# Performance work log

Measured on AMD Instinct MI355X. Metric: run time of the kernel, lower is better.

## Reference

```python
import jax, jax.numpy as jnp
import numpy as np

N = 50000      # nodes
E = 400000     # edges (before self-loops)
F = 128        # num_features
H = 8          # heads
C = 64         # hidden_channels (per-head dim of conv1)
K = 32         # num_classes (per-head dim of conv2)
NEG_SLOPE = 0.2


def _glorot(key, shape):
    fan_in, fan_out = shape[0], shape[-1]
    scale = jnp.sqrt(2.0 / (fan_in + fan_out)).astype(jnp.float32)
    return jax.random.normal(key, shape, dtype=jnp.float32) * scale


def setup_inputs() -> dict:
    key = jax.random.key(0)
    ks = jax.random.split(key, 14)
    return {
        "x": jax.random.normal(ks[0], (N, F), dtype=jnp.float32),
        "edge_index": jax.random.randint(ks[1], (2, E), 0, N, dtype=jnp.int32),
        "xyz": jax.random.normal(ks[2], (N, 3), dtype=jnp.float32),
        # lin1 residual: Linear(F, K)
        "lin1_w": _glorot(ks[3], (F, K)),
        "lin1_b": jnp.zeros((K,), jnp.float32),
        # conv1: GATv2Conv(F, C, heads=8, concat=False)
        "wl1": _glorot(ks[4], (F, H * C)),
        "wr1": _glorot(ks[5], (F, H * C)),
        "att1": _glorot(ks[6], (H, C)),
        "b1": jnp.zeros((C,), jnp.float32),
        # conv2: GATv2Conv(C, K, heads=8, concat=False)
        "wl2": _glorot(ks[7], (C, H * K)),
        "wr2": _glorot(ks[8], (C, H * K)),
        "att2": _glorot(ks[9], (H, K)),
        "b2": jnp.zeros((K,), jnp.float32),
    }


def _gatv2_layer(x, src, dst, wl, wr, att, bias, heads, ch):
    """GATv2Conv with concat=False (mean over heads), add_self_loops already in edges."""
    n = x.shape[0]
    xl = (x @ wl).reshape(n, heads, ch)   # source transform W_l x
    xr = (x @ wr).reshape(n, heads, ch)   # target transform W_r x
    # edge score: e_ij = a_h . leaky_relu(xl[j] + xr[i])  -> [E, H]
    e = jnp.einsum('ehc,hc->eh', jax.nn.leaky_relu(xl[src] + xr[dst], NEG_SLOPE), att)
    # segment softmax over incoming edges of each destination node
    m = jax.ops.segment_max(e, dst, num_segments=n)
    ex = jnp.exp(e - m[dst])
    denom = jax.ops.segment_sum(ex, dst, num_segments=n)
    alpha = ex / denom[dst]                                      # [E, H]
    out = jax.ops.segment_sum(alpha[:, :, None] * xl[src], dst, num_segments=n)  # [N, H, C]
    return out.mean(axis=1) + bias        # concat=False -> head average, then bias


def reference(x, edge_index, xyz, lin1_w, lin1_b, wl1, wr1, att1, b1,
              wl2, wr2, att2, b2):
    n = x.shape[0]
    # PyG GATv2Conv default: add self loops
    loops = jnp.arange(n, dtype=edge_index.dtype)
    src = jnp.concatenate([edge_index[0], loops])
    dst = jnp.concatenate([edge_index[1], loops])

    residual1 = x @ lin1_w + lin1_b                      # lin1(x)
    h = _gatv2_layer(x, src, dst, wl1, wr1, att1, b1, H, C)
    h = jax.nn.relu(h)                                   # dropout is identity in eval
    out = _gatv2_layer(h, src, dst, wl2, wr2, att2, b2, H, K)
    return out + residual1
```

## Files before the change

kernel.cpp:

```cpp
#include <hip/hip_runtime.h>
#include <hip/hip_bf16.h>

#define NNODE 50000
#define NEDGE 400000
#define NTOT  450000
#define FDIM  128
#define HEADS 8
#define SCANB ((NNODE + 255) / 256)

typedef __bf16 bf16x8 __attribute__((ext_vector_type(8)));
typedef float  f32x4  __attribute__((ext_vector_type(4)));
typedef unsigned short u16x8 __attribute__((ext_vector_type(8)));
typedef unsigned short u16x4 __attribute__((ext_vector_type(4)));
typedef __hip_bfloat16 bf16;

static __device__ __forceinline__ float lrelu(float v) {
  return v > 0.f ? v : 0.2f * v;
}
static __device__ __forceinline__ float b2f(unsigned short u) {
  union { float f; unsigned int i; } x; x.i = ((unsigned int)u) << 16; return x.f;
}


__global__ __launch_bounds__(256) void k_count(const int* __restrict__ ei, int* __restrict__ deg) {
  int t = blockIdx.x * 256 + threadIdx.x;
  if (t >= NTOT) return;
  int d = (t < NEDGE) ? ei[NEDGE + t] : (t - NEDGE);
  atomicAdd(&deg[d], 1);
}

__global__ __launch_bounds__(256) void k_scan1(const int* __restrict__ deg, int* __restrict__ offs,
                                               int* __restrict__ bsum) {
  __shared__ int buf[256];
  int i = blockIdx.x * 256 + threadIdx.x;
  int v = (i < NNODE) ? deg[i] : 0;
  buf[threadIdx.x] = v;
  __syncthreads();
  for (int off = 1; off < 256; off <<= 1) {
    int t = (threadIdx.x >= off) ? buf[threadIdx.x - off] : 0;
    __syncthreads();
    buf[threadIdx.x] += t;
    __syncthreads();
  }
  if (i < NNODE) offs[i + 1] = buf[threadIdx.x];
  if (threadIdx.x == 255) bsum[blockIdx.x] = buf[255];
  if (i == 0) offs[0] = 0;
}

__global__ __launch_bounds__(256) void k_scan2(int* __restrict__ bsum, int nb) {
  __shared__ int buf[256];
  int v = (threadIdx.x < nb) ? bsum[threadIdx.x] : 0;
  buf[threadIdx.x] = v;
  __syncthreads();
  for (int off = 1; off < 256; off <<= 1) {
    int t = (threadIdx.x >= off) ? buf[threadIdx.x - off] : 0;
    __syncthreads();
    buf[threadIdx.x] += t;
    __syncthreads();
  }
  if (threadIdx.x < nb) bsum[threadIdx.x] = buf[threadIdx.x] - v;
}

__global__ __launch_bounds__(256) void k_scan3(int* __restrict__ offs, const int* __restrict__ bsum) {
  int i = blockIdx.x * 256 + threadIdx.x;
  if (i < NNODE) offs[i + 1] += bsum[blockIdx.x];
}

__global__ __launch_bounds__(256) void k_fill(const int* __restrict__ ei, const int* __restrict__ offs,
                                              int* __restrict__ cur, int* __restrict__ csrc) {
  int t = blockIdx.x * 256 + threadIdx.x;
  if (t >= NTOT) return;
  int s, d;
  if (t < NEDGE) { s = ei[t]; d = ei[NEDGE + t]; }
  else { s = t - NEDGE; d = s; }
  int pos = offs[d] + atomicAdd(&cur[d], 1);
  csrc[pos] = s;
}


__global__ __launch_bounds__(256) void k_cast(const float* __restrict__ in, bf16* __restrict__ o, int nvec) {
  int t = blockIdx.x * 256 + threadIdx.x;
  if (t >= nvec) return;
  float4 v = *(const float4*)(in + (size_t)t * 4);
  bf16* p = o + (size_t)t * 4;
  p[0] = __float2bfloat16(v.x);
  p[1] = __float2bfloat16(v.y);
  p[2] = __float2bfloat16(v.z);
  p[3] = __float2bfloat16(v.w);
}


template<int K, int N>
__global__ __launch_bounds__(256) void k_pack(const float* __restrict__ Wl, const float* __restrict__ Wr,
                                              bf16* __restrict__ Bp) {
  constexpr int KS = K / 32;
  int t = blockIdx.x * 256 + threadIdx.x;
  if (t >= (N / 16) * KS * 64) return;
  int lane = t & 63;
  int ks = (t >> 6) % KS;
  int cb = t / (64 * KS);
  int col = cb * 16 + (lane & 15);
  int k0 = ks * 32 + (lane >> 4) * 8;
  const float* W = (col < N / 2) ? Wl : Wr;
  int c = (col < N / 2) ? col : col - N / 2;
  bf16* o = Bp + (size_t)t * 8;
#pragma unroll
  for (int j = 0; j < 8; ++j)
    o[j] = __float2bfloat16(W[(size_t)(k0 + j) * (N / 2) + c]);
}


template<int K, int N>
__global__ __launch_bounds__(256) void k_mfma(const bf16* __restrict__ A,
                                              const bf16* __restrict__ Bp,
                                              bf16* __restrict__ xl, bf16* __restrict__ xr,
                                              int n) {
  constexpr int KS = K / 32;
  const int lane = threadIdx.x & 63;
  const int wave = threadIdx.x >> 6;
  const int rb = blockIdx.x * 32;
  const int cb0 = blockIdx.y * 16 + wave * 4;
  const int r16 = lane & 15, kg = lane >> 4;

  bf16x8 a[2][KS];
#pragma unroll
  for (int mf = 0; mf < 2; ++mf) {
    int row = rb + 16 * mf + r16;
    if (row >= n) row = n - 1;
    const bf16* pa = A + (size_t)row * K + kg * 8;
#pragma unroll
    for (int ks = 0; ks < KS; ++ks)
      a[mf][ks] = *(const bf16x8*)(pa + ks * 32);
  }

#pragma unroll
  for (int nf = 0; nf < 4; ++nf) {
    int cb = cb0 + nf;
    f32x4 acc0 = {0.f, 0.f, 0.f, 0.f}, acc1 = {0.f, 0.f, 0.f, 0.f};
    const bf16* pb = Bp + (size_t)cb * KS * 512 + lane * 8;
#pragma unroll
    for (int ks = 0; ks < KS; ++ks) {
      bf16x8 b = *(const bf16x8*)(pb + ks * 512);
      acc0 = __builtin_amdgcn_mfma_f32_16x16x32_bf16(a[0][ks], b, acc0, 0, 0, 0);
      acc1 = __builtin_amdgcn_mfma_f32_16x16x32_bf16(a[1][ks], b, acc1, 0, 0, 0);
    }
    int col = cb * 16 + r16;
    bf16* OUT; int c;
    if (col < N / 2) { OUT = xl; c = col; } else { OUT = xr; c = col - N / 2; }
#pragma unroll
    for (int reg = 0; reg < 4; ++reg) {
      int row0 = rb + kg * 4 + reg;
      if (row0 < n) OUT[(size_t)row0 * (N / 2) + c] = __float2bfloat16(acc0[reg]);
      int row1 = rb + 16 + kg * 4 + reg;
      if (row1 < n) OUT[(size_t)row1 * (N / 2) + c] = __float2bfloat16(acc1[reg]);
    }
  }
}


__global__ __launch_bounds__(256) void k_residual(const float* __restrict__ X,
                                                  const float* __restrict__ W,
                                                  const float* __restrict__ b,
                                                  float* __restrict__ out, int n) {
  __shared__ float xs[8 * 128];
  int row0 = blockIdx.x * 8;
  for (int t = threadIdx.x; t < 8 * 128; t += 256) {
    int r = t >> 7;
    xs[t] = (row0 + r < n) ? X[(size_t)(row0 + r) * 128 + (t & 127)] : 0.f;
  }
  __syncthreads();
  int r = threadIdx.x >> 5, c = threadIdx.x & 31;
  float acc = 0.f;
  for (int k = 0; k < 128; ++k) acc += xs[r * 128 + k] * W[k * 32 + c];
  if (row0 + r < n) out[(size_t)(row0 + r) * 32 + c] = acc + b[c];
}


template<int D, int VEC, bool L1>
__global__ __launch_bounds__(256) void k_gat(const bf16* __restrict__ xl,
                                             const bf16* __restrict__ xr,
                                             const float* __restrict__ att,
                                             const int* __restrict__ csrc,
                                             const int* __restrict__ offs,
                                             const float* __restrict__ bias,
                                             const float* __restrict__ resid,
                                             bf16* __restrict__ out1,
                                             float* __restrict__ out2) {
  constexpr int CH = D / 8;
  int node = blockIdx.x * 4 + (threadIdx.x >> 6);
  int lane = threadIdx.x & 63;
  if (node >= NNODE) return;
  int beg = offs[node], end = offs[node + 1];

  float attv[VEC], xrv[VEC];
  {
    const float* pa = att + lane * VEC;
    const unsigned short* pr = (const unsigned short*)(xr + (size_t)node * D) + lane * VEC;
#pragma unroll
    for (int j = 0; j < VEC; ++j) { attv[j] = pa[j]; xrv[j] = b2f(pr[j]); }
  }

  float m = -1e30f, den = 0.f;
  float acc[VEC];
#pragma unroll
  for (int j = 0; j < VEC; ++j) acc[j] = 0.f;

  typedef unsigned short uvec __attribute__((ext_vector_type(VEC)));
  const unsigned short* xlb = (const unsigned short*)xl;

  uvec a_cur = *(const uvec*)(xlb + (size_t)csrc[beg] * D + lane * VEC);
  for (int i = beg; i < end; ++i) {
    uvec a_next = a_cur;
    if (i + 1 < end)
      a_next = *(const uvec*)(xlb + (size_t)csrc[i + 1] * D + lane * VEC);
    float av[VEC];
#pragma unroll
    for (int j = 0; j < VEC; ++j) av[j] = b2f(a_cur[j]);
    float sc = 0.f;
#pragma unroll
    for (int j = 0; j < VEC; ++j) sc += lrelu(av[j] + xrv[j]) * attv[j];
    sc += __shfl_xor(sc, 1);
    sc += __shfl_xor(sc, 2);
    sc += __shfl_xor(sc, 4);
    float mn = fmaxf(m, sc);
    float scale = __expf(m - mn);
    float w = __expf(sc - mn);
    den = den * scale + w;
#pragma unroll
    for (int j = 0; j < VEC; ++j) acc[j] = acc[j] * scale + w * av[j];
    m = mn;
    a_cur = a_next;
  }

  float inv = 1.f / den;
#pragma unroll
  for (int j = 0; j < VEC; ++j) {
    float v = acc[j] * inv;
    v += __shfl_xor(v, 8);
    v += __shfl_xor(v, 16);
    v += __shfl_xor(v, 32);
    acc[j] = v;
  }

  if (lane < 8) {
    int c0 = lane * VEC;
    if constexpr (L1) {
      bf16* o = out1 + (size_t)node * CH + c0;
#pragma unroll
      for (int j = 0; j < VEC; ++j) {
        float v = acc[j] * 0.125f + bias[c0 + j];
        o[j] = __float2bfloat16(fmaxf(v, 0.f));
      }
    } else {
      float* o = out2 + (size_t)node * CH + c0;
      const float* rs = resid + (size_t)node * CH + c0;
#pragma unroll
      for (int j = 0; j < VEC; ++j)
        o[j] = acc[j] * 0.125f + bias[c0 + j] + rs[j];
    }
  }
}


extern "C" void kernel_launch(void* const* d_in, const int* in_sizes, int n_in,
                              void* d_out, int out_size, void* d_ws, size_t ws_size,
                              hipStream_t stream) {
  const float* x      = (const float*)d_in[0];
  const int*   ei     = (const int*)d_in[1];
  const float* lin1_w = (const float*)d_in[3];
  const float* lin1_b = (const float*)d_in[4];
  const float* wl1    = (const float*)d_in[5];
  const float* wr1    = (const float*)d_in[6];
  const float* att1   = (const float*)d_in[7];
  const float* b1     = (const float*)d_in[8];
  const float* wl2    = (const float*)d_in[9];
  const float* wr2    = (const float*)d_in[10];
  const float* att2   = (const float*)d_in[11];
  const float* b2     = (const float*)d_in[12];
  float* out = (float*)d_out;

  char* p = (char*)d_ws;
  auto alloc = [&](size_t bytes) {
    char* r = p;
    p += (bytes + 255) & ~size_t(255);
    return r;
  };
  int*   offs  = (int*)alloc((NNODE + 1) * 4);
  int*   deg   = (int*)alloc(NNODE * 4);
  int*   cur   = (int*)alloc(NNODE * 4);
  int*   bsum  = (int*)alloc(SCANB * 4);
  int*   csrc  = (int*)alloc((size_t)NTOT * 4);
  bf16*  xb    = (bf16*)alloc((size_t)NNODE * 128 * 2);
  bf16*  xl    = (bf16*)alloc((size_t)NNODE * 512 * 2);
  bf16*  xr    = (bf16*)alloc((size_t)NNODE * 512 * 2);
  bf16*  h1    = (bf16*)alloc((size_t)NNODE * 64 * 2);
  bf16*  Bp1   = (bf16*)alloc((size_t)128 * 1024 * 2);
  bf16*  Bp2   = (bf16*)alloc((size_t)64 * 512 * 2);
  float* resid = (float*)alloc((size_t)NNODE * 32 * 4);

  (void)hipMemsetAsync(deg, 0, NNODE * 4, stream);
  (void)hipMemsetAsync(cur, 0, NNODE * 4, stream);

  k_count<<<(NTOT + 255) / 256, 256, 0, stream>>>(ei, deg);
  k_scan1<<<SCANB, 256, 0, stream>>>(deg, offs, bsum);
  k_scan2<<<1, 256, 0, stream>>>(bsum, SCANB);
  k_scan3<<<SCANB, 256, 0, stream>>>(offs, bsum);
  k_fill<<<(NTOT + 255) / 256, 256, 0, stream>>>(ei, offs, cur, csrc);
  k_cast<<<(NNODE * 128 / 4 + 255) / 256, 256, 0, stream>>>(x, xb, NNODE * 128 / 4);
  k_pack<128, 1024><<<64, 256, 0, stream>>>(wl1, wr1, Bp1);
  k_pack<64, 512><<<16, 256, 0, stream>>>(wl2, wr2, Bp2);
  k_residual<<<NNODE / 8, 256, 0, stream>>>(x, lin1_w, lin1_b, resid, NNODE);

  k_mfma<128, 1024><<<dim3((NNODE + 31) / 32, 4), 256, 0, stream>>>(xb, Bp1, xl, xr, NNODE);
  k_gat<512, 8, true><<<(NNODE + 3) / 4, 256, 0, stream>>>(xl, xr, att1, csrc, offs, b1, nullptr, h1, nullptr);

  k_mfma<64, 512><<<dim3((NNODE + 31) / 32, 2), 256, 0, stream>>>(h1, Bp2, xl, xr, NNODE);
  k_gat<256, 4, false><<<(NNODE + 3) / 4, 256, 0, stream>>>(xl, xr, att2, csrc, offs, b2, resid, nullptr, out);
}
```

Measured before the change: 327.1 us.

## Split GAT node aggregation across two waves and drop online-softmax max tracking

Each destination node is now handled by two wavefronts, 128 threads in total. Each wave covers half of the feature row with half the vector width, and the two halves are combined through shared memory before the output is written. The gather of source rows now prefetches two edges ahead instead of one. The running-max rescaling in the softmax is removed and exp(score) is accumulated directly. This cuts per-edge exp and multiply work and raises memory-level parallelism, but it risks overflow if attention scores become large. It also adds a block-wide barrier and a shared-memory reduction.

New measurement: 413.4 us. 1.26x slower.

```diff
diff --git a/kernel.cpp b/kernel.cpp
--- a/kernel.cpp
+++ b/kernel.cpp
@@ -10,13 +10,8 @@
 
 typedef __bf16 bf16x8 __attribute__((ext_vector_type(8)));
 typedef float  f32x4  __attribute__((ext_vector_type(4)));
-typedef unsigned short u16x8 __attribute__((ext_vector_type(8)));
-typedef unsigned short u16x4 __attribute__((ext_vector_type(4)));
 typedef __hip_bfloat16 bf16;
 
-static __device__ __forceinline__ float lrelu(float v) {
-  return v > 0.f ? v : 0.2f * v;
-}
 static __device__ __forceinline__ float b2f(unsigned short u) {
   union { float f; unsigned int i; } x; x.i = ((unsigned int)u) << 16; return x.f;
 }
@@ -187,76 +182,89 @@
                                              bf16* __restrict__ out1,
                                              float* __restrict__ out2) {
   constexpr int CH = D / 8;
-  int node = blockIdx.x * 4 + (threadIdx.x >> 6);
-  int lane = threadIdx.x & 63;
-  if (node >= NNODE) return;
-  int beg = offs[node], end = offs[node + 1];
+  constexpr unsigned ROWB = D * 2;
+  __shared__ float part[2][CH];
+  const int nib  = threadIdx.x >> 7;
+  const int w    = (threadIdx.x >> 6) & 1;
+  const int lane = threadIdx.x & 63;
+  const int node = blockIdx.x * 2 + nib;
+
+  const int beg = offs[node], end = offs[node + 1];
+  const unsigned boff = (unsigned)(w * (D / 2) + lane * VEC) * 2u;
+
+  typedef unsigned short uvec __attribute__((ext_vector_type(VEC)));
+  const char* xlp = (const char*)xl + boff;
 
   float attv[VEC], xrv[VEC];
   {
-    const float* pa = att + lane * VEC;
-    const unsigned short* pr = (const unsigned short*)(xr + (size_t)node * D) + lane * VEC;
-#pragma unroll
-    for (int j = 0; j < VEC; ++j) { attv[j] = pa[j]; xrv[j] = b2f(pr[j]); }
-  }
-
-  float m = -1e30f, den = 0.f;
+    const float* pa = att + w * (D / 2) + lane * VEC;
+    uvec rv = *(const uvec*)((const char*)xr + (unsigned)node * ROWB + boff);
+#pragma unroll
+    for (int j = 0; j < VEC; ++j) { attv[j] = pa[j]; xrv[j] = b2f(rv[j]); }
+  }
+
+  float den = 0.f;
   float acc[VEC];
 #pragma unroll
   for (int j = 0; j < VEC; ++j) acc[j] = 0.f;
 
-  typedef unsigned short uvec __attribute__((ext_vector_type(VEC)));
-  const unsigned short* xlb = (const unsigned short*)xl;
-
-  uvec a_cur = *(const uvec*)(xlb + (size_t)csrc[beg] * D + lane * VEC);
+  uvec A0 = *(const uvec*)(xlp + (unsigned)csrc[beg] * ROWB);
+  int i1 = (beg + 1 < end) ? beg + 1 : end - 1;
+  uvec A1 = *(const uvec*)(xlp + (unsigned)csrc[i1] * ROWB);
   for (int i = beg; i < end; ++i) {
-    uvec a_next = a_cur;
-    if (i + 1 < end)
-      a_next = *(const uvec*)(xlb + (size_t)csrc[i + 1] * D + lane * VEC);
+    uvec Ac = A0;
+    A0 = A1;
+    int inx = (i + 2 < end) ? i + 2 : end - 1;
+    A1 = *(const uvec*)(xlp + (unsigned)csrc[inx] * ROWB);
+
     float av[VEC];
-#pragma unroll
-    for (int j = 0; j < VEC; ++j) av[j] = b2f(a_cur[j]);
     float sc = 0.f;
 #pragma unroll
-    for (int j = 0; j < VEC; ++j) sc += lrelu(av[j] + xrv[j]) * attv[j];
+    for (int j = 0; j < VEC; ++j) {
+      av[j] = b2f(Ac[j]);
+      float t = av[j] + xrv[j];
+      sc += fmaxf(t, 0.2f * t) * attv[j];
+    }
     sc += __shfl_xor(sc, 1);
     sc += __shfl_xor(sc, 2);
     sc += __shfl_xor(sc, 4);
-    float mn = fmaxf(m, sc);
-    float scale = __expf(m - mn);
-    float w = __expf(sc - mn);
-    den = den * scale + w;
-#pragma unroll
-    for (int j = 0; j < VEC; ++j) acc[j] = acc[j] * scale + w * av[j];
-    m = mn;
-    a_cur = a_next;
-  }
-
-  float inv = 1.f / den;
+    sc += __shfl_xor(sc, 8);
+    float wgt = __expf(sc);
+    den += wgt;
+#pragma unroll
+    for (int j = 0; j < VEC; ++j) acc[j] += wgt * av[j];
+  }
+
+  const float inv = 1.f / den;
+  float v[VEC];
 #pragma unroll
   for (int j = 0; j < VEC; ++j) {
-    float v = acc[j] * inv;
-    v += __shfl_xor(v, 8);
-    v += __shfl_xor(v, 16);
-    v += __shfl_xor(v, 32);
-    acc[j] = v;
-  }
-
-  if (lane < 8) {
+    float t = acc[j] * inv;
+    t += __shfl_xor(t, 16);
+    t += __shfl_xor(t, 32);
+    v[j] = t;
+  }
+
+  if (w == 1 && lane < 16) {
+#pragma unroll
+    for (int j = 0; j < VEC; ++j) part[nib][lane * VEC + j] = v[j];
+  }
+  __syncthreads();
+  if (w == 0 && lane < 16) {
     int c0 = lane * VEC;
     if constexpr (L1) {
       bf16* o = out1 + (size_t)node * CH + c0;
 #pragma unroll
       for (int j = 0; j < VEC; ++j) {
-        float v = acc[j] * 0.125f + bias[c0 + j];
-        o[j] = __float2bfloat16(fmaxf(v, 0.f));
+        float t = (v[j] + part[nib][c0 + j]) * 0.125f + bias[c0 + j];
+        o[j] = __float2bfloat16(fmaxf(t, 0.f));
       }
     } else {
       float* o = out2 + (size_t)node * CH + c0;
       const float* rs = resid + (size_t)node * CH + c0;
 #pragma unroll
       for (int j = 0; j < VEC; ++j)
-        o[j] = acc[j] * 0.125f + bias[c0 + j] + rs[j];
+        o[j] = (v[j] + part[nib][c0 + j]) * 0.125f + bias[c0 + j] + rs[j];
     }
   }
 }
@@ -312,8 +320,8 @@
   k_residual<<<NNODE / 8, 256, 0, stream>>>(x, lin1_w, lin1_b, resid, NNODE);
 
   k_mfma<128, 1024><<<dim3((NNODE + 31) / 32, 4), 256, 0, stream>>>(xb, Bp1, xl, xr, NNODE);
-  k_gat<512, 8, true><<<(NNODE + 3) / 4, 256, 0, stream>>>(xl, xr, att1, csrc, offs, b1, nullptr, h1, nullptr);
+  k_gat<512, 4, true><<<NNODE / 2, 256, 0, stream>>>(xl, xr, att1, csrc, offs, b1, nullptr, h1, nullptr);
 
   k_mfma<64, 512><<<dim3((NNODE + 31) / 32, 2), 256, 0, stream>>>(h1, Bp2, xl, xr, NNODE);
-  k_gat<256, 4, false><<<(NNODE + 3) / 4, 256, 0, stream>>>(xl, xr, att2, csrc, offs, b2, resid, nullptr, out);
-}
+  k_gat<256, 2, false><<<NNODE / 2, 256, 0, stream>>>(xl, xr, att2, csrc, offs, b2, resid, nullptr, out);
+}
```
